# Optimization experiments

Measured on AMD Instinct MI355X. Metric: run time of the kernel, lower is better.

Reference implementation:

```python
import jax, jax.numpy as jnp
import numpy as np
from jax import lax


def setup_inputs() -> dict:
    key = jax.random.key(0)
    k = jax.random.split(key, 5)
    B, T = 16384, 1024
    return {
        "x": jax.random.normal(k[0], (B, T, 1), dtype=jnp.float32),
        # PyTorch LSTM param layout: [4*hidden, input] with gate order i, f, g, o
        "w_ih": jax.random.normal(k[1], (4, 1), dtype=jnp.float32),
        "w_hh": jax.random.normal(k[2], (4, 1), dtype=jnp.float32),
        "b_ih": jax.random.normal(k[3], (4,), dtype=jnp.float32),
        "b_hh": jax.random.normal(k[4], (4,), dtype=jnp.float32),
    }


def reference(x, w_ih, w_hh, b_ih, b_hh):
    # x: [B, T, 1]; single-layer unidirectional LSTM with hidden_size=1,
    # zero initial state (model resets hidden each forward).
    B = x.shape[0]
    h0 = jnp.zeros((B, 1), dtype=x.dtype)
    c0 = jnp.zeros((B, 1), dtype=x.dtype)
    b = b_ih + b_hh  # [4]

    def step(carry, xt):
        h, c = carry  # [B,1] each
        gates = xt @ w_ih.T + h @ w_hh.T + b  # [B,4], gate order i,f,g,o
        i, f, g, o = jnp.split(gates, 4, axis=-1)
        i = jax.nn.sigmoid(i)
        f = jax.nn.sigmoid(f)
        g = jnp.tanh(g)
        o = jax.nn.sigmoid(o)
        c_new = f * c + i * g
        h_new = o * jnp.tanh(c_new)
        return (h_new, c_new), h_new

    xs = jnp.swapaxes(x, 0, 1)  # [T, B, 1]
    _, ys = lax.scan(step, (h0, c0), xs)  # ys: [T, B, 1]
    return jnp.swapaxes(ys, 0, 1)  # [B, T, 1]
```

## Files before the change

kernel.cpp:

```cpp
#include <hip/hip_runtime.h>


#define LOG2E 1.44269504088896340736f

typedef float __attribute__((ext_vector_type(4))) f32x4;

__global__ __launch_bounds__(64) void lstm_h1_kernel(
    const float* __restrict__ x,
    const float* __restrict__ w_ih,
    const float* __restrict__ w_hh,
    const float* __restrict__ b_ih,
    const float* __restrict__ b_hh,
    float* __restrict__ out,
    int B, int T)
{
    __shared__ float lds[64][17];

    const int lane    = (int)threadIdx.x;
    const int bid     = blockIdx.x;
    const int chunk   = bid & 3;
    const int rowblk  = bid >> 2;
    const int rowbase = rowblk * 64;
    const int row     = rowbase + lane;
    if (row >= B) return;

    const float b0 = b_ih[0] + b_hh[0];
    const float b1 = b_ih[1] + b_hh[1];
    const float b2 = b_ih[2] + b_hh[2];
    const float b3 = b_ih[3] + b_hh[3];

    const float ciw = -LOG2E * w_ih[0],        cib = -LOG2E * b0,        cih = -LOG2E * w_hh[0];
    const float cfw = -LOG2E * w_ih[1],        cfb = -LOG2E * b1,        cfh = -LOG2E * w_hh[1];
    const float cgw = -2.0f * LOG2E * w_ih[2], cgb = -2.0f * LOG2E * b2, cgh = -2.0f * LOG2E * w_hh[2];
    const float cow = -LOG2E * w_ih[3],        cob = -LOG2E * b3,        coh = -LOG2E * w_hh[3];
    const float n2L = -2.0f * LOG2E;

    const float c2ih = 2.0f * cih, c2fh = 2.0f * cfh, c2gh = 2.0f * cgh, c2oh = 2.0f * coh;

    float rc = 0.5f, cs = 0.0f, so = 0.0f;

    const f32x4* __restrict__ xr4 = reinterpret_cast<const f32x4*>(x + (size_t)row * T);

    const int gs  = 56 * chunk;
    const int ssu = chunk ? 8 : 0;
    const int t0  = gs * 4;

    const f32x4* __restrict__ xg = xr4 + gs;

#define LSTM_STEP(xx, hout)                                                   \
    {                                                                         \
        const float _x = (xx);                                                \
        float ai = fmaf(_x, ciw, cib);                                        \
        float af = fmaf(_x, cfw, cfb);                                        \
        float ag = fmaf(_x, cgw, cgb);                                        \
        float ao = fmaf(_x, cow, cob);                                        \
        float p2i = c2ih * so, p2f = c2fh * so, p2g = c2gh * so, p2o = c2oh * so; \
        float ami = fmaf(cih, -so, ai);                                       \
        float amf = fmaf(cfh, -so, af);                                       \
        float amg = fmaf(cgh, -so, ag);                                       \
        float amo = fmaf(coh, -so, ao);                                       \
        float ui = fmaf(rc, p2i, ami);                                        \
        float uf = fmaf(rc, p2f, amf);                                        \
        float ug = fmaf(rc, p2g, amg);                                        \
        float uo = fmaf(rc, p2o, amo);                                        \
        float Ei = __builtin_amdgcn_exp2f(ui);                                \
        float Ef = __builtin_amdgcn_exp2f(uf);                                \
        float Eg = __builtin_amdgcn_exp2f(ug);                                \
        float Eo = __builtin_amdgcn_exp2f(uo);                                \
        float di = 1.0f + Ei;                                                 \
        float df = 1.0f + Ef;                                                 \
        float dg = 1.0f + Eg;                                                 \
        float dd = 1.0f + Eo;                                                 \
        float dgdf = dg * df;                                                 \
        float csdg = cs * dg;                                                 \
        float nt   = fmaf(n2L, -Eg, n2L);                     \
        float ntdf = nt * df;                                                 \
        float D2   = di * dgdf;                                               \
        float csD  = csdg * di;                                               \
        float num  = csD + ntdf;                                              \
        float Q2   = __builtin_amdgcn_rcpf(D2);                               \
        so = __builtin_amdgcn_rcpf(dd);                \
        cs = num * Q2;                                                        \
        float Ec = __builtin_amdgcn_exp2f(cs);                                \
        float dc = 1.0f + Ec;                                                 \
        rc = __builtin_amdgcn_rcpf(dc);                                       \
        float tc = fmaf(2.0f, rc, -1.0f);                                     \
        (hout) = so * tc;                                                     \
    }

#define GROUP(bufv, g)                                                        \
    {                                                                         \
        f32x4 hv;                                                             \
        LSTM_STEP((bufv)[0], hv[0]);                                          \
        LSTM_STEP((bufv)[1], hv[1]);                                          \
        LSTM_STEP((bufv)[2], hv[2]);                                          \
        LSTM_STEP((bufv)[3], hv[3]);                                          \
        lds[lane][4*(g)+0] = hv[0]; lds[lane][4*(g)+1] = hv[1];               \
        lds[lane][4*(g)+2] = hv[2]; lds[lane][4*(g)+3] = hv[3];               \
    }

#define STOREPH(u)                                                            \
    {                                                                         \
        const int _r = (lane >> 2);                                           \
        const int _c = 4 * (lane & 3);                                        \
        const int _t = t0 + (u) * 16 + _c;                                    \
        _Pragma("unroll")                                                     \
        for (int _s = 0; _s < 4; ++_s) {                                      \
            const int _row = 16 * _s + _r;                                    \
            f32x4 _vv;                                                        \
            _vv[0] = lds[_row][_c + 0];                                       \
            _vv[1] = lds[_row][_c + 1];                                       \
            _vv[2] = lds[_row][_c + 2];                                       \
            _vv[3] = lds[_row][_c + 3];                                       \
            *reinterpret_cast<f32x4*>(out + (size_t)(rowbase + _row) * T + _t) = _vv; \
        }                                                                     \
    }

#define UNIT(u, V0, V1, V2, V3)                                               \
    {                                                                         \
        GROUP(V0, 0); GROUP(V1, 1); GROUP(V2, 2); GROUP(V3, 3);               \
        if ((u) >= ssu) STOREPH(u);                                           \
    }

    f32x4 a0, a1, a2, a3, q0, q1, q2, q3;

    a0 = xg[0]; a1 = xg[1]; a2 = xg[2]; a3 = xg[3];

    for (int it = 0; it < 11; ++it) {
        const int uA = 2 * it, uB = 2 * it + 1;

        {
            const f32x4* p = xg + uB * 4;
            q0 = p[0]; q1 = p[1]; q2 = p[2]; q3 = p[3];
        }
        __builtin_amdgcn_sched_barrier(0);

        UNIT(uA, a0, a1, a2, a3);

        {
            const int un = (uB + 1 < 22) ? (uB + 1) : 21;
            const f32x4* p = xg + un * 4;
            a0 = p[0]; a1 = p[1]; a2 = p[2]; a3 = p[3];
        }
        __builtin_amdgcn_sched_barrier(0);

        UNIT(uB, q0, q1, q2, q3);
    }

#undef UNIT
#undef STOREPH
#undef GROUP
#undef LSTM_STEP
}

extern "C" void kernel_launch(void* const* d_in, const int* in_sizes, int n_in,
                              void* d_out, int out_size, void* d_ws, size_t ws_size,
                              hipStream_t stream) {
    const float* x    = (const float*)d_in[0];
    const float* w_ih = (const float*)d_in[1];
    const float* w_hh = (const float*)d_in[2];
    const float* b_ih = (const float*)d_in[3];
    const float* b_hh = (const float*)d_in[4];
    float* out = (float*)d_out;

    const int T = 1024;
    const int B = in_sizes[0] / T;

    const int block = 64;
    const int grid = ((B + 63) / 64) * 4;
    lstm_h1_kernel<<<grid, block, 0, stream>>>(x, w_ih, w_hh, b_ih, b_hh, out, B, T);
}
```

Before: 44.56 us.

## Track cell state as a rational fraction and approximate tanh with a Padé form

Reformulates the LSTM step so the cell state is carried as an unnormalized numerator/denominator pair, rescaled by an exponent trick, instead of being divided each step. tanh(c) is computed with a rational Padé approximant on a clamped argument rather than exp2 plus reciprocal. This removes one exp2 and two reciprocals from the serial dependency chain per step, in exchange for more FMAs. The clamp at |c|<=5 and the Padé approximation change numerical accuracy for large cell values.

```diff
diff --git a/kernel.cpp b/kernel.cpp
--- a/kernel.cpp
+++ b/kernel.cpp
@@ -33,11 +33,8 @@
     const float cfw = -LOG2E * w_ih[1],        cfb = -LOG2E * b1,        cfh = -LOG2E * w_hh[1];
     const float cgw = -2.0f * LOG2E * w_ih[2], cgb = -2.0f * LOG2E * b2, cgh = -2.0f * LOG2E * w_hh[2];
     const float cow = -LOG2E * w_ih[3],        cob = -LOG2E * b3,        coh = -LOG2E * w_hh[3];
-    const float n2L = -2.0f * LOG2E;
 
-    const float c2ih = 2.0f * cih, c2fh = 2.0f * cfh, c2gh = 2.0f * cgh, c2oh = 2.0f * coh;
-
-    float rc = 0.5f, cs = 0.0f, so = 0.0f;
+    float nS = 0.0f, dS = 1.0f, hh = 0.0f;
 
     const f32x4* __restrict__ xr4 = reinterpret_cast<const f32x4*>(x + (size_t)row * T);
 
@@ -54,15 +51,10 @@
         float af = fmaf(_x, cfw, cfb);                                        \
         float ag = fmaf(_x, cgw, cgb);                                        \
         float ao = fmaf(_x, cow, cob);                                        \
-        float p2i = c2ih * so, p2f = c2fh * so, p2g = c2gh * so, p2o = c2oh * so; \
-        float ami = fmaf(cih, -so, ai);                                       \
-        float amf = fmaf(cfh, -so, af);                                       \
-        float amg = fmaf(cgh, -so, ag);                                       \
-        float amo = fmaf(coh, -so, ao);                                       \
-        float ui = fmaf(rc, p2i, ami);                                        \
-        float uf = fmaf(rc, p2f, amf);                                        \
-        float ug = fmaf(rc, p2g, amg);                                        \
-        float uo = fmaf(rc, p2o, amo);                                        \
+        float ui = fmaf(hh, cih, ai);                                         \
+        float uf = fmaf(hh, cfh, af);                                         \
+        float ug = fmaf(hh, cgh, ag);                                         \
+        float uo = fmaf(hh, coh, ao);                                         \
         float Ei = __builtin_amdgcn_exp2f(ui);                                \
         float Ef = __builtin_amdgcn_exp2f(uf);                                \
         float Eg = __builtin_amdgcn_exp2f(ug);                                \
@@ -71,21 +63,36 @@
         float df = 1.0f + Ef;                                                 \
         float dg = 1.0f + Eg;                                                 \
         float dd = 1.0f + Eo;                                                 \
-        float dgdf = dg * df;                                                 \
-        float csdg = cs * dg;                                                 \
-        float nt   = fmaf(n2L, -Eg, n2L);                     \
-        float ntdf = nt * df;                                                 \
-        float D2   = di * dgdf;                                               \
-        float csD  = csdg * di;                                               \
-        float num  = csD + ntdf;                                              \
-        float Q2   = __builtin_amdgcn_rcpf(D2);                               \
-        so = __builtin_amdgcn_rcpf(dd);                \
-        cs = num * Q2;                                                        \
-        float Ec = __builtin_amdgcn_exp2f(cs);                                \
-        float dc = 1.0f + Ec;                                                 \
-        rc = __builtin_amdgcn_rcpf(dc);                                       \
-        float tc = fmaf(2.0f, rc, -1.0f);                                     \
-        (hout) = so * tc;                                                     \
+        float didg = di * dg;                                                 \
+        float omg  = 1.0f - Eg;                                               \
+        float w2   = omg * df;                                                \
+        float t1   = dS * w2;                                                 \
+        float nT   = fmaf(nS, didg, t1);                                      \
+        float dgdf = didg * df;                                               \
+        float dT   = dS * dgdf;                                               \
+        unsigned ke = __float_as_uint(dT) & 0x7f800000u;                      \
+        float rs = __uint_as_float(0x7f000000u - ke);         \
+        float hi5 = 5.0f * dT;                                                \
+        float nCl = fmaxf(-hi5, fminf(nT, hi5));         \
+        float nC = nCl * rs;                                                  \
+        float dN = dT * rs;                                     \
+        nS = nT * rs;                                                         \
+        dS = dN;                                                              \
+        float _v  = dN * dN;                                                  \
+        float _w  = nC * nC;                                                  \
+        float _v2 = _v * _v;                                                  \
+        float _v3 = _v2 * _v;                                                 \
+        float _p1 = fmaf(_w, 21.0f, 1260.0f * _v);                            \
+        float _P  = fmaf(_p1, _w, 10395.0f * _v2);                            \
+        float _q1 = fmaf(_v, 210.0f, _w);                                     \
+        float _q2 = fmaf(_q1, _w, 4725.0f * _v2);                             \
+        float _Q  = fmaf(_q2, _w, 10395.0f * _v3);                            \
+        float _nd = nC * dN;                                                  \
+        float _nP = _nd * _P;                                                 \
+        float _QQ = _Q * dd;                                                  \
+        float _rq = __builtin_amdgcn_rcpf(_QQ);                               \
+        hh = _nP * _rq;                         \
+        (hout) = hh;                                                          \
     }
 
 #define GROUP(bufv, g)                                                        \
```

After: 49.09 us. +10.2%, slower.
